# Optimization experiments

Measured on AMD Instinct MI355X. Metric: run time of the kernel, lower is better.

## Reference

```python
import jax, jax.numpy as jnp
import numpy as np

H = 256  # hidden size of nn.RNN(1, 256)


def setup_inputs() -> dict:
    key = jax.random.key(0)
    k1, k2, k3, k4, k5 = jax.random.split(key, 5)
    B, T = 4096, 256
    bound = 1.0 / np.sqrt(H)  # PyTorch RNN default init: U(-1/sqrt(H), 1/sqrt(H))
    return {
        "T": T,
        "flat_img": jax.random.normal(k1, (B, T), dtype=jnp.float32),
        "W_ih": jax.random.uniform(k2, (H, 1), minval=-bound, maxval=bound, dtype=jnp.float32),
        "W_hh": jax.random.uniform(k3, (H, H), minval=-bound, maxval=bound, dtype=jnp.float32),
        "b_ih": jax.random.uniform(k4, (H,), minval=-bound, maxval=bound, dtype=jnp.float32),
        "b_hh": jax.random.uniform(k5, (H,), minval=-bound, maxval=bound, dtype=jnp.float32),
    }


def reference(T, flat_img, W_ih, W_hh, b_ih, b_hh):
    B = flat_img.shape[0]
    dtype = flat_img.dtype
    latent0 = jnp.zeros((1, B, H), dtype)

    # timestep = arange(T, 0, -1); t_prime = T - t runs 0..T-1 in loop order
    ts = jnp.arange(T, 0, -1).astype(dtype)
    a_t = (ts + 1.0) / (T + 1.0)
    sigmas = jnp.sqrt(a_t * (1.0 - a_t))          # [T]
    xs = flat_img[:, :T].T                         # [T, B], row i is flat_img[:, t_prime=i]
    noise_keys = jax.random.split(jax.random.key(42), T)

    w_ih = W_ih[:, 0]                              # input_size == 1 -> matvec is a broadcast

    def step(latent, inp):
        x_t, sigma_t, k = inp
        x = x_t[None, :, None]                     # [1, B, 1]
        # single RNN-tanh step: tanh(x W_ih^T + b_ih + h W_hh^T + b_hh)
        h = jnp.tanh(x * w_ih + b_ih + jnp.einsum('lbh,gh->lbg', latent, W_hh) + b_hh)
        eps = 0.1 * jax.random.normal(k, latent.shape, dtype)
        latent = latent + x + h + sigma_t * eps    # x broadcasts [1,B,1]->[1,B,H]
        return latent, None

    latent, _ = jax.lax.scan(step, latent0, (xs, sigmas, noise_keys))
    return latent
```

## Files before the change

### kernel.cpp

```cpp
#include <hip/hip_runtime.h>


#define TSTEPS 256
#define HDIM   256
#define ROWS   16
#define LSTR   264
#define TILE   (ROWS * LSTR)
#define XSTR   260

typedef _Float16 half8 __attribute__((ext_vector_type(8)));
typedef __attribute__((ext_vector_type(4))) float float4v;

struct U2 { unsigned x, y; };

__device__ __forceinline__ void tfround(unsigned &x0, unsigned &x1, const int r) {
  x0 += x1;
  x1 = __builtin_rotateleft32(x1, r);
  x1 ^= x0;
}

__device__ __forceinline__ U2 threefry(unsigned k0, unsigned k1, unsigned x0, unsigned x1) {
  unsigned k2 = k0 ^ k1 ^ 0x1BD11BDAu;
  x0 += k0; x1 += k1;
  tfround(x0,x1,13); tfround(x0,x1,15); tfround(x0,x1,26); tfround(x0,x1,6);
  x0 += k1; x1 += k2 + 1u;
  tfround(x0,x1,17); tfround(x0,x1,29); tfround(x0,x1,16); tfround(x0,x1,24);
  x0 += k2; x1 += k0 + 2u;
  tfround(x0,x1,13); tfround(x0,x1,15); tfround(x0,x1,26); tfround(x0,x1,6);
  x0 += k0; x1 += k1 + 3u;
  tfround(x0,x1,17); tfround(x0,x1,29); tfround(x0,x1,16); tfround(x0,x1,24);
  x0 += k1; x1 += k2 + 4u;
  tfround(x0,x1,13); tfround(x0,x1,15); tfround(x0,x1,26); tfround(x0,x1,6);
  x0 += k2; x1 += k0 + 5u;
  return {x0, x1};
}

__device__ __forceinline__ float jax_normal_from_bits(unsigned bits) {
#pragma clang fp contract(off)
  const float LO = __builtin_bit_cast(float, 0xBF7FFFFFu);
  float f = __builtin_bit_cast(float, (bits >> 9) | 0x3f800000u) - 1.0f;
  float u = fmaf(f, 2.0f, LO);
  u = fmaxf(u, LO);
  float t1 = u * u;
  float s  = 1.0f - t1;
  float w  = -0.6931471805599453f * __builtin_amdgcn_logf(s);
  float p;
  if (w < 5.0f) {
    float z = w - 2.5f;
    p = 2.81022636e-08f;
    p = fmaf(p, z, 3.43273939e-07f);
    p = fmaf(p, z, -3.5233877e-06f);
    p = fmaf(p, z, -4.39150654e-06f);
    p = fmaf(p, z, 0.00021858087f);
    p = fmaf(p, z, -0.00125372503f);
    p = fmaf(p, z, -0.00417768164f);
    p = fmaf(p, z, 0.246640727f);
    p = fmaf(p, z, 1.50140941f);
  } else {
    float z = sqrtf(w) - 3.0f;
    p = -0.000200214257f;
    p = fmaf(p, z, 0.000100950558f);
    p = fmaf(p, z, 0.00134934322f);
    p = fmaf(p, z, -0.00367342844f);
    p = fmaf(p, z, 0.00573950773f);
    p = fmaf(p, z, -0.0076224613f);
    p = fmaf(p, z, 0.00943887047f);
    p = fmaf(p, z, 1.00167406f);
    p = fmaf(p, z, 2.83297682f);
  }
  return 1.4142135623730951f * (p * u);
}

__device__ __forceinline__ float4v mfma_f16(half8 a, half8 b, float4v c) {
  return __builtin_amdgcn_mfma_f32_16x16x32_f16(a, b, c, 0, 0, 0);
}

__global__ __launch_bounds__(256, 8)
void drnet_rng(float* __restrict__ nws) {
  const unsigned bid = blockIdx.x;
  const unsigned t   = bid >> 6;
  U2 kk = threefry(0u, 42u, 0u, t);
  unsigned kA = (unsigned)__builtin_amdgcn_readfirstlane((int)kk.x);
  unsigned kB = (unsigned)__builtin_amdgcn_readfirstlane((int)kk.y);
  const unsigned base = bid * 16384u + threadIdx.x * 4u;
  #pragma unroll 4
  for (unsigned s = 0; s < 16; ++s) {
    unsigned e0 = base + (s << 10);
    unsigned b0 = ((e0 >> 12) & 255u) * 16u + ((e0 >> 6) & 3u) * 4u;
    unsigned g  = ((e0 >> 8) & 15u) * 16u + ((e0 >> 2) & 15u);
    unsigned j0 = b0 * 256u + g;
    float4v v;
    #pragma unroll
    for (int r = 0; r < 4; ++r) {
      U2 rr = threefry(kA, kB, 0u, j0 + ((unsigned)r << 8));
      v[r] = jax_normal_from_bits(rr.x ^ rr.y);
    }
    *(float4v*)(nws + e0) = v;
  }
}

__global__ __launch_bounds__(1024, 4)
void drnet_scan(const float* __restrict__ flat_img,
                const float* __restrict__ W_ih,
                const float* __restrict__ W_hh,
                const float* __restrict__ b_ih,
                const float* __restrict__ b_hh,
                const float* __restrict__ nws,
                float* __restrict__ out)
{
  __shared__ __align__(16) char lds_pool[86016];
  float* x_sh = (float*)lds_pool;
  short* latp = (short*)(lds_pool + 16640);

  const int tid  = threadIdx.x;
  const int wg   = blockIdx.x;
  const int wv   = tid >> 6;
  const int lane = tid & 63;
  const int q    = lane >> 4;
  const int c    = lane & 15;

  {
    int i = tid * 4;
    int m = i >> 8;
    float4v v = *(const float4v*)(flat_img + (size_t)wg * (ROWS*TSTEPS) + i);
    *(float4v*)&x_sh[m * XSTR + (i & 255)] = v;
  }
  {
    int* p0 = (int*)latp;
    for (int i = tid; i < 2 * TILE; i += 1024) p0[i] = 0;
  }

  half8 Wh[8], Wl[8];
  const int g = wv*16 + c;
  const float bias = b_ih[g] + b_hh[g];
  const float wih  = W_ih[g];
  #pragma unroll
  for (int kk = 0; kk < 8; ++kk) {
    const float* wp = W_hh + g*HDIM + kk*32 + q*8;
    float4v w0 = *(const float4v*)wp;
    float4v w1 = *(const float4v*)(wp + 4);
    half8 h8, l8;
    #pragma unroll
    for (int j2 = 0; j2 < 4; ++j2) {
      float f0 = w0[j2], f1 = w1[j2];
      _Float16 h0 = (_Float16)f0, h1 = (_Float16)f1;
      _Float16 l0 = (_Float16)((f0 - (float)h0) * 2048.0f);
      _Float16 l1 = (_Float16)((f1 - (float)h1) * 2048.0f);
      h8[j2] = h0; h8[j2+4] = h1;
      l8[j2] = l0; l8[j2+4] = l1;
    }
    Wh[kk] = h8; Wl[kk] = l8;
  }

  float lat[4] = {0.f, 0.f, 0.f, 0.f};
  const unsigned jbase = ((unsigned)(wg*ROWS + q*4) << 8) + (unsigned)g;
  const int aoff = c * LSTR + q * 8;
  const int woff = (q*4) * LSTR + wv*16 + c;

  const float4v* np = (const float4v*)nws + ((unsigned)wg*1024u + (unsigned)wv*64u + (unsigned)lane);
  float4v nz_pend = np[0];

  __syncthreads();

  for (int t = 0; t < TSTEPS; ++t) {
    float4v nz = nz_pend;
    {
      int tn = t + 1 < TSTEPS ? t + 1 : t;
      nz_pend = np[(size_t)tn * 262144u];
    }

    float tsf = (float)(TSTEPS - t);
    float a_t = (tsf + 1.0f) / 257.0f;
    float escale = 0.1f * sqrtf(a_t * (1.0f - a_t));

    const short* rb = latp + (t & 1) * (2*TILE) + aoff;
    short*       wb = latp + ((t + 1) & 1) * (2*TILE) + woff;

    float4v aa = {0.f, 0.f, 0.f, 0.f};
    float4v ab = {0.f, 0.f, 0.f, 0.f};
    #pragma unroll
    for (int kk = 0; kk < 8; ++kk) {
      half8 ah = *(const half8*)(rb + 0*TILE + kk*32);
      half8 al = *(const half8*)(rb + 1*TILE + kk*32);
      aa = mfma_f16(ah, Wh[kk], aa);
      ab = mfma_f16(al, Wh[kk], ab);
      ab = mfma_f16(ah, Wl[kk], ab);
    }

    #pragma unroll
    for (int r = 0; r < 4; ++r) lat[r] = fmaf(escale, nz[r], lat[r]);

    float xr[4];
    #pragma unroll
    for (int r = 0; r < 4; ++r) xr[r] = x_sh[(q*4 + r) * XSTR + t];

    #pragma unroll
    for (int r = 0; r < 4; ++r) {
      float d = aa[r] + ab[r] * (1.0f / 2048.0f);
      float pre = d + fmaf(xr[r], wih, bias);
      float h;
      if (__builtin_fabsf(pre) >= 7.90531110763549805f) {
        h = pre > 0.0f ? 1.0f : -1.0f;
      } else {
        float e = __builtin_amdgcn_exp2f(pre * 2.8853900817779268f);
        h = fmaf(-2.0f, __builtin_amdgcn_rcpf(e + 1.0f), 1.0f);
      }
      float nl = lat[r] + xr[r] + h;
      lat[r] = nl;
      _Float16 hh = (_Float16)nl;
      _Float16 ll = (_Float16)((nl - (float)hh) * 2048.0f);
      short* wp = wb + r*LSTR;
      wp[0]    = __builtin_bit_cast(short, hh);
      wp[TILE] = __builtin_bit_cast(short, ll);
    }
    __syncthreads();
  }

  #pragma unroll
  for (int r = 0; r < 4; ++r)
    out[jbase + (unsigned)(r << 8)] = lat[r];
}

__global__ __launch_bounds__(1024, 4)
void drnet_fused(const float* __restrict__ flat_img,
                 const float* __restrict__ W_ih,
                 const float* __restrict__ W_hh,
                 const float* __restrict__ b_ih,
                 const float* __restrict__ b_hh,
                 float* __restrict__ out)
{
  __shared__ __align__(16) char lds_pool[86016];
  float*    x_sh    = (float*)lds_pool;
  unsigned* keys_sh = (unsigned*)(lds_pool + 16640);
  short*    latp    = (short*)(lds_pool + 18688);

  const int tid  = threadIdx.x;
  const int wg   = blockIdx.x;
  const int wv   = tid >> 6;
  const int lane = tid & 63;
  const int q    = lane >> 4;
  const int c    = lane & 15;

  if (tid < TSTEPS) {
    U2 kk = threefry(0u, 42u, 0u, (unsigned)tid);
    keys_sh[2*tid]   = kk.x;
    keys_sh[2*tid+1] = kk.y;
  }
  {
    int i = tid * 4;
    int m = i >> 8;
    float4v v = *(const float4v*)(flat_img + (size_t)wg * (ROWS*TSTEPS) + i);
    *(float4v*)&x_sh[m * XSTR + (i & 255)] = v;
  }
  {
    int* p0 = (int*)latp;
    for (int i = tid; i < 2 * TILE; i += 1024) p0[i] = 0;
  }

  half8 Wh[8], Wl[8];
  const int g = wv*16 + c;
  const float bias = b_ih[g] + b_hh[g];
  const float wih  = W_ih[g];
  #pragma unroll
  for (int kk = 0; kk < 8; ++kk) {
    const float* wp = W_hh + g*HDIM + kk*32 + q*8;
    float4v w0 = *(const float4v*)wp;
    float4v w1 = *(const float4v*)(wp + 4);
    half8 h8, l8;
    #pragma unroll
    for (int j2 = 0; j2 < 4; ++j2) {
      float f0 = w0[j2], f1 = w1[j2];
      _Float16 h0 = (_Float16)f0, h1 = (_Float16)f1;
      _Float16 l0 = (_Float16)((f0 - (float)h0) * 2048.0f);
      _Float16 l1 = (_Float16)((f1 - (float)h1) * 2048.0f);
      h8[j2] = h0; h8[j2+4] = h1;
      l8[j2] = l0; l8[j2+4] = l1;
    }
    Wh[kk] = h8; Wl[kk] = l8;
  }

  float lat[4] = {0.f, 0.f, 0.f, 0.f};
  const unsigned jbase = ((unsigned)(wg*ROWS + q*4) << 8) + (unsigned)g;
  const int aoff = c * LSTR + q * 8;
  const int woff = (q*4) * LSTR + wv*16 + c;

  __syncthreads();

  for (int t = 0; t < TSTEPS; ++t) {
    unsigned kA = (unsigned)__builtin_amdgcn_readfirstlane((int)keys_sh[2*t]);
    unsigned kB = (unsigned)__builtin_amdgcn_readfirstlane((int)keys_sh[2*t+1]);

    float tsf = (float)(TSTEPS - t);
    float a_t = (tsf + 1.0f) / 257.0f;
    float escale = 0.1f * sqrtf(a_t * (1.0f - a_t));

    const short* rb = latp + (t & 1) * (2*TILE) + aoff;
    short*       wb = latp + ((t + 1) & 1) * (2*TILE) + woff;

    float4v aa = {0.f, 0.f, 0.f, 0.f};
    float4v ab = {0.f, 0.f, 0.f, 0.f};
    #pragma unroll
    for (int kk = 0; kk < 8; ++kk) {
      half8 ah = *(const half8*)(rb + 0*TILE + kk*32);
      half8 al = *(const half8*)(rb + 1*TILE + kk*32);
      aa = mfma_f16(ah, Wh[kk], aa);
      ab = mfma_f16(al, Wh[kk], ab);
      ab = mfma_f16(ah, Wl[kk], ab);
      if (kk < 4) {
        unsigned j = jbase + (unsigned)(kk << 8);
        U2 rr = threefry(kA, kB, 0u, j);
        float nrm = jax_normal_from_bits(rr.x ^ rr.y);
        lat[kk] = fmaf(escale, nrm, lat[kk]);
      }
    }

    float xr[4];
    #pragma unroll
    for (int r = 0; r < 4; ++r) xr[r] = x_sh[(q*4 + r) * XSTR + t];

    #pragma unroll
    for (int r = 0; r < 4; ++r) {
      float d = aa[r] + ab[r] * (1.0f / 2048.0f);
      float pre = d + fmaf(xr[r], wih, bias);
      float h;
      if (__builtin_fabsf(pre) >= 7.90531110763549805f) {
        h = pre > 0.0f ? 1.0f : -1.0f;
      } else {
        float e = __builtin_amdgcn_exp2f(pre * 2.8853900817779268f);
        h = fmaf(-2.0f, __builtin_amdgcn_rcpf(e + 1.0f), 1.0f);
      }
      float nl = lat[r] + xr[r] + h;
      lat[r] = nl;
      _Float16 hh = (_Float16)nl;
      _Float16 ll = (_Float16)((nl - (float)hh) * 2048.0f);
      short* wp = wb + r*LSTR;
      wp[0]    = __builtin_bit_cast(short, hh);
      wp[TILE] = __builtin_bit_cast(short, ll);
    }
    __syncthreads();
  }

  #pragma unroll
  for (int r = 0; r < 4; ++r)
    out[jbase + (unsigned)(r << 8)] = lat[r];
}

extern "C" void kernel_launch(void* const* d_in, const int* in_sizes, int n_in,
                              void* d_out, int out_size, void* d_ws, size_t ws_size,
                              hipStream_t stream) {
  (void)in_sizes; (void)n_in; (void)out_size;
  const float* flat_img = (const float*)d_in[1];
  const float* W_ih     = (const float*)d_in[2];
  const float* W_hh     = (const float*)d_in[3];
  const float* b_ih     = (const float*)d_in[4];
  const float* b_hh     = (const float*)d_in[5];
  const size_t need = (size_t)268435456 * 4;
  if (ws_size >= need) {
    drnet_rng<<<dim3(16384), dim3(256), 0, stream>>>((float*)d_ws);
    drnet_scan<<<dim3(4096 / ROWS), dim3(1024), 0, stream>>>(
        flat_img, W_ih, W_hh, b_ih, b_hh, (const float*)d_ws, (float*)d_out);
  } else {
    drnet_fused<<<dim3(4096 / ROWS), dim3(1024), 0, stream>>>(
        flat_img, W_ih, W_hh, b_ih, b_hh, (float*)d_out);
  }
}
```

Measured before the change: 989.4 us.

## Chunk noise generation and scan into 32-step slabs to shrink workspace

Rather than pre-generating all 256 timesteps of noise (1 GiB) and then running one scan, the host loops over 8 chunks. Each chunk generates 32 timesteps of noise into a 128 MiB slab, then runs a scan kernel over those steps. The latent state is saved to and restored from workspace between chunks. The smaller slab may stay resident in the large last-level cache instead of streaming through HBM, at the cost of 16 launches, repeated weight/x setup, and re-quantizing the latent on every chunk restart.

```diff
diff --git a/kernel.cpp b/kernel.cpp
--- a/kernel.cpp
+++ b/kernel.cpp
@@ -7,6 +7,7 @@
 #define LSTR   264
 #define TILE   (ROWS * LSTR)
 #define XSTR   260
+#define SCH    32
 
 typedef _Float16 half8 __attribute__((ext_vector_type(8)));
 typedef __attribute__((ext_vector_type(4))) float float4v;
@@ -75,17 +76,18 @@
   return __builtin_amdgcn_mfma_f32_16x16x32_f16(a, b, c, 0, 0, 0);
 }
 
-__global__ __launch_bounds__(256, 8)
-void drnet_rng(float* __restrict__ nws) {
+__global__ __launch_bounds__(256, 4)
+void drnet_rng(float* __restrict__ slab, int t0) {
   const unsigned bid = blockIdx.x;
-  const unsigned t   = bid >> 6;
-  U2 kk = threefry(0u, 42u, 0u, t);
+  const unsigned ts  = bid >> 6;
+  U2 kk = threefry(0u, 42u, 0u, (unsigned)t0 + ts);
   unsigned kA = (unsigned)__builtin_amdgcn_readfirstlane((int)kk.x);
   unsigned kB = (unsigned)__builtin_amdgcn_readfirstlane((int)kk.y);
-  const unsigned base = bid * 16384u + threadIdx.x * 4u;
-  #pragma unroll 4
+  const unsigned e20 = (bid & 63u) * 16384u + threadIdx.x * 4u;
+  float* dst = slab + ((size_t)ts << 20);
+  #pragma unroll 2
   for (unsigned s = 0; s < 16; ++s) {
-    unsigned e0 = base + (s << 10);
+    unsigned e0 = e20 + (s << 10);
     unsigned b0 = ((e0 >> 12) & 255u) * 16u + ((e0 >> 6) & 3u) * 4u;
     unsigned g  = ((e0 >> 8) & 15u) * 16u + ((e0 >> 2) & 15u);
     unsigned j0 = b0 * 256u + g;
@@ -95,18 +97,20 @@
       U2 rr = threefry(kA, kB, 0u, j0 + ((unsigned)r << 8));
       v[r] = jax_normal_from_bits(rr.x ^ rr.y);
     }
-    *(float4v*)(nws + e0) = v;
+    *(float4v*)(dst + e0) = v;
   }
 }
 
 __global__ __launch_bounds__(1024, 4)
-void drnet_scan(const float* __restrict__ flat_img,
-                const float* __restrict__ W_ih,
-                const float* __restrict__ W_hh,
-                const float* __restrict__ b_ih,
-                const float* __restrict__ b_hh,
-                const float* __restrict__ nws,
-                float* __restrict__ out)
+void drnet_scan32(const float* __restrict__ flat_img,
+                  const float* __restrict__ W_ih,
+                  const float* __restrict__ W_hh,
+                  const float* __restrict__ b_ih,
+                  const float* __restrict__ b_hh,
+                  const float* __restrict__ slab,
+                  float* __restrict__ latsave,
+                  float* __restrict__ out,
+                  int t0, int first, int last)
 {
   __shared__ __align__(16) char lds_pool[86016];
   float* x_sh = (float*)lds_pool;
@@ -125,13 +129,30 @@
     float4v v = *(const float4v*)(flat_img + (size_t)wg * (ROWS*TSTEPS) + i);
     *(float4v*)&x_sh[m * XSTR + (i & 255)] = v;
   }
-  {
+
+  const int g = wv*16 + c;
+  float lat[4] = {0.f, 0.f, 0.f, 0.f};
+  const unsigned jbase = ((unsigned)(wg*ROWS + q*4) << 8) + (unsigned)g;
+  const int aoff = c * LSTR + q * 8;
+  const int woff = (q*4) * LSTR + wv*16 + c;
+
+  if (first) {
     int* p0 = (int*)latp;
     for (int i = tid; i < 2 * TILE; i += 1024) p0[i] = 0;
+  } else {
+    #pragma unroll
+    for (int r = 0; r < 4; ++r) {
+      float nl = latsave[jbase + ((unsigned)r << 8)];
+      lat[r] = nl;
+      _Float16 hh = (_Float16)nl;
+      _Float16 ll = (_Float16)((nl - (float)hh) * 2048.0f);
+      short* wp = latp + woff + r*LSTR;
+      wp[0]    = __builtin_bit_cast(short, hh);
+      wp[TILE] = __builtin_bit_cast(short, ll);
+    }
   }
 
   half8 Wh[8], Wl[8];
-  const int g = wv*16 + c;
   const float bias = b_ih[g] + b_hh[g];
   const float wih  = W_ih[g];
   #pragma unroll
@@ -152,29 +173,24 @@
     Wh[kk] = h8; Wl[kk] = l8;
   }
 
-  float lat[4] = {0.f, 0.f, 0.f, 0.f};
-  const unsigned jbase = ((unsigned)(wg*ROWS + q*4) << 8) + (unsigned)g;
-  const int aoff = c * LSTR + q * 8;
-  const int woff = (q*4) * LSTR + wv*16 + c;
-
-  const float4v* np = (const float4v*)nws + ((unsigned)wg*1024u + (unsigned)wv*64u + (unsigned)lane);
+  const float4v* np = (const float4v*)slab +
+      ((unsigned)wg*1024u + (unsigned)wv*64u + (unsigned)lane);
   float4v nz_pend = np[0];
 
   __syncthreads();
 
-  for (int t = 0; t < TSTEPS; ++t) {
+  for (int ts = 0; ts < SCH; ++ts) {
     float4v nz = nz_pend;
-    {
-      int tn = t + 1 < TSTEPS ? t + 1 : t;
-      nz_pend = np[(size_t)tn * 262144u];
-    }
-
+    int tn = ts + 1 < SCH ? ts + 1 : ts;
+    nz_pend = np[(size_t)tn * 262144u];
+
+    int t = t0 + ts;
     float tsf = (float)(TSTEPS - t);
     float a_t = (tsf + 1.0f) / 257.0f;
     float escale = 0.1f * sqrtf(a_t * (1.0f - a_t));
 
-    const short* rb = latp + (t & 1) * (2*TILE) + aoff;
-    short*       wb = latp + ((t + 1) & 1) * (2*TILE) + woff;
+    const short* rb = latp + (ts & 1) * (2*TILE) + aoff;
+    short*       wb = latp + ((ts + 1) & 1) * (2*TILE) + woff;
 
     float4v aa = {0.f, 0.f, 0.f, 0.f};
     float4v ab = {0.f, 0.f, 0.f, 0.f};
@@ -216,9 +232,13 @@
     __syncthreads();
   }
 
-  #pragma unroll
-  for (int r = 0; r < 4; ++r)
-    out[jbase + (unsigned)(r << 8)] = lat[r];
+  if (last) {
+    #pragma unroll
+    for (int r = 0; r < 4; ++r) out[jbase + ((unsigned)r << 8)] = lat[r];
+  } else {
+    #pragma unroll
+    for (int r = 0; r < 4; ++r) latsave[jbase + ((unsigned)r << 8)] = lat[r];
+  }
 }
 
 __global__ __launch_bounds__(1024, 4)
@@ -354,11 +374,16 @@
   const float* W_hh     = (const float*)d_in[3];
   const float* b_ih     = (const float*)d_in[4];
   const float* b_hh     = (const float*)d_in[5];
-  const size_t need = (size_t)268435456 * 4;
+  const size_t need = ((size_t)SCH << 20) * 4 + ((size_t)1 << 22);
   if (ws_size >= need) {
-    drnet_rng<<<dim3(16384), dim3(256), 0, stream>>>((float*)d_ws);
-    drnet_scan<<<dim3(4096 / ROWS), dim3(1024), 0, stream>>>(
-        flat_img, W_ih, W_hh, b_ih, b_hh, (const float*)d_ws, (float*)d_out);
+    float* latsave = (float*)d_ws;
+    float* slab    = latsave + (1u << 20);
+    for (int ch = 0; ch < TSTEPS / SCH; ++ch) {
+      drnet_rng<<<dim3(SCH * 64), dim3(256), 0, stream>>>(slab, ch * SCH);
+      drnet_scan32<<<dim3(4096 / ROWS), dim3(1024), 0, stream>>>(
+          flat_img, W_ih, W_hh, b_ih, b_hh, slab, latsave, (float*)d_out,
+          ch * SCH, ch == 0, ch == (TSTEPS / SCH - 1));
+    }
   } else {
     drnet_fused<<<dim3(4096 / ROWS), dim3(1024), 0, stream>>>(
         flat_img, W_ih, W_hh, b_ih, b_hh, (float*)d_out);
```

Result: slower. 1.227 ms (+24.0%).
